# Kernel optimization log

Measured on AMD Instinct MI355X. Metric: run time of the kernel, lower is better.

## Reference

```python
import jax, jax.numpy as jnp
import numpy as np
from jax import lax

B, T, F = 8, 512, 128          # batch, mel time, mel freq
DM, DS, DC, EXP, NL = 384, 16, 4, 2, 12
DI = EXP * DM                   # 768 inner width
DTR = (DM + 15) // 16           # 24, mamba_ssm dt_rank='auto'
PT = PF = 16
L = (T // PT) * (F // PF)       # 256 patches
NC = 4


def setup_inputs() -> dict:
    key = jax.random.key(0)
    ks = iter(jax.random.split(key, 24))
    def n(shape, s=0.02):
        return jax.random.normal(next(ks), shape, jnp.float32) * s
    return {
        "x": jax.random.normal(next(ks), (B, T, F), jnp.float32),
        "patch_w": n((DM, PT, PF)),
        "patch_b": jnp.zeros((DM,), jnp.float32),
        "pos_embed": n((1, L, DM)),
        "ln_g": jnp.ones((NL, DM), jnp.float32),
        "ln_b": jnp.zeros((NL, DM), jnp.float32),
        "in_proj_w": n((NL, 2 * DI, DM)),
        "conv_w": n((NL, DI, DC), 0.1),
        "conv_b": jnp.zeros((NL, DI), jnp.float32),
        "x_proj_w": n((NL, DTR + 2 * DS, DI)),
        "dt_proj_w": n((NL, DI, DTR), 0.1),
        "dt_proj_b": n((NL, DI), 0.1),
        "A_log": jnp.tile(jnp.log(jnp.arange(1, DS + 1, dtype=jnp.float32))[None, None, :], (NL, DI, 1)),
        "Dskip": jnp.ones((NL, DI), jnp.float32),
        "out_proj_w": n((NL, DM, DI)),
        "fn_g": jnp.ones((DM,), jnp.float32),
        "fn_b": jnp.zeros((DM,), jnp.float32),
        "head_w": n((NC, DM)),
        "head_b": jnp.zeros((NC,), jnp.float32),
    }


def _layernorm(x, g, b):
    m = x.mean(-1, keepdims=True)
    v = jnp.var(x, axis=-1, keepdims=True)
    return (x - m) * lax.rsqrt(v + 1e-5) * g + b


def _silu(v):
    return v * jax.nn.sigmoid(v)


def _mamba_block(x, p):
    # x: [B, L, DM]; residual Mamba block (pre-LN, dropout=identity in eval)
    ln_g, ln_b, Wi, cw, cb, Wx, Wdt, bdt, A_log, Dsk, Wo = p
    res = x
    h = _layernorm(x, ln_g, ln_b)
    xz = jnp.einsum('bld,ed->ble', h, Wi)          # [B,L,2*DI]
    u, z = jnp.split(xz, 2, axis=-1)
    # causal depthwise conv1d, kernel DC (small, unrolled)
    up = jnp.pad(u, ((0, 0), (DC - 1, 0), (0, 0)))
    u = sum(up[:, k:k + L, :] * cw[:, k] for k in range(DC)) + cb
    u = _silu(u)
    proj = jnp.einsum('bld,ed->ble', u, Wx)        # [B,L,DTR+2*DS]
    dt, Bm, Cm = jnp.split(proj, [DTR, DTR + DS], axis=-1)
    delta = jax.nn.softplus(jnp.einsum('blr,dr->bld', dt, Wdt) + bdt)  # [B,L,DI]
    A = -jnp.exp(A_log)                            # [DI, DS]
    dA = jnp.exp(delta[..., None] * A)             # [B,L,DI,DS]
    dBu = (delta * u)[..., None] * Bm[:, :, None, :]

    def step(hst, inp):
        dA_t, dBu_t, C_t = inp
        hst = dA_t * hst + dBu_t                   # [B,DI,DS]
        return hst, jnp.einsum('bdn,bn->bd', hst, C_t)

    h0 = jnp.zeros((x.shape[0], DI, DS), x.dtype)
    _, ys = lax.scan(step, h0, (dA.swapaxes(0, 1), dBu.swapaxes(0, 1), Cm.swapaxes(0, 1)))
    y = ys.swapaxes(0, 1) + u * Dsk                # [B,L,DI]
    y = y * _silu(z)
    return res + jnp.einsum('bld,ed->ble', y, Wo)


def reference(x, patch_w, patch_b, pos_embed, ln_g, ln_b, in_proj_w, conv_w, conv_b,
              x_proj_w, dt_proj_w, dt_proj_b, A_log, Dskip, out_proj_w,
              fn_g, fn_b, head_w, head_b):
    Bn = x.shape[0]
    # patch embed = non-overlapping 16x16 conv == blocked reshape + einsum
    patches = x.reshape(Bn, T // PT, PT, F // PF, PF)
    tok = jnp.einsum('bhpwq,dpq->bhwd', patches, patch_w) + patch_b
    tok = tok.reshape(Bn, L, DM) + pos_embed

    def layer(carry, p):
        return _mamba_block(carry, p), None

    tok, _ = lax.scan(layer, tok, (ln_g, ln_b, in_proj_w, conv_w, conv_b,
                                   x_proj_w, dt_proj_w, dt_proj_b, A_log, Dskip, out_proj_w))
    tok = _layernorm(tok, fn_g, fn_b)
    pooled = tok.mean(axis=1)
    return pooled @ head_w.T + head_b
```

## Files before the change

kernel.cpp:

```cpp
#include <hip/hip_runtime.h>
#include <math.h>

namespace {

constexpr int kB   = 8;
constexpr int kL   = 256;
constexpr int kTok = 2048;
constexpr int kDM  = 384;
constexpr int kDI  = 768;
constexpr int kDS  = 16;
constexpr int kDTR = 24;
constexpr int kPROJ = 56;
constexpr int kNL  = 12;

constexpr int kWIN  = 2 * kDI * kDM;
constexpr int kWOUT = kDM * kDI;
constexpr int kWX   = kPROJ * kDI;
constexpr int kWTOT = kWIN + kWOUT + kWX;

typedef float f32x4 __attribute__((ext_vector_type(4)));
typedef short short8 __attribute__((ext_vector_type(8)));

__device__ __forceinline__ float softplus_f(float x) {
  return (x > 20.f) ? x : log1pf(__expf(x));
}
__device__ __forceinline__ float silu_f(float x) {
  return x / (1.f + __expf(-x));
}
__device__ __forceinline__ unsigned short f2bf(float f) {
  union { float f; unsigned u; } v; v.f = f;
  unsigned r = v.u + 0x7FFFu + ((v.u >> 16) & 1u);
  return (unsigned short)(r >> 16);
}
__device__ __forceinline__ float bf2f(unsigned short u) {
  return __uint_as_float((unsigned)u << 16);
}

__global__ __launch_bounds__(256) void patch_gemm_k(
    const float* __restrict__ x, const float* __restrict__ Bw,
    const float* __restrict__ bias, const float* __restrict__ pos,
    float* __restrict__ C) {
  __shared__ float As[16][68];
  __shared__ float Bs[16][68];
  int tid = threadIdx.x;
  int bm = blockIdx.y * 64;
  int bn = blockIdx.x * 64;
  int lr = tid >> 2;
  int lk = (tid & 3) << 2;
  int tm = (tid >> 4) << 2;
  int tn = (tid & 15) << 2;
  float acc[4][4] = {};
  for (int k0 = 0; k0 < 256; k0 += 16) {
    {
      int token = bm + lr;
      int b = token >> 8, l = token & 255;
      int h = l >> 3, w = l & 7;
      int p = k0 >> 4;
      const float* ap = x + ((size_t)(b * 512) + h * 16 + p) * 128 + w * 16 + lk;
      float4 av = *(const float4*)ap;
      As[lk + 0][lr] = av.x; As[lk + 1][lr] = av.y;
      As[lk + 2][lr] = av.z; As[lk + 3][lr] = av.w;
    }
    {
      const float* bp = Bw + (size_t)(bn + lr) * 256 + k0 + lk;
      float4 bv = *(const float4*)bp;
      Bs[lk + 0][lr] = bv.x; Bs[lk + 1][lr] = bv.y;
      Bs[lk + 2][lr] = bv.z; Bs[lk + 3][lr] = bv.w;
    }
    __syncthreads();
    #pragma unroll
    for (int k = 0; k < 16; ++k) {
      float4 a = *(const float4*)&As[k][tm];
      float4 b = *(const float4*)&Bs[k][tn];
      float av[4] = {a.x, a.y, a.z, a.w};
      float bv[4] = {b.x, b.y, b.z, b.w};
      #pragma unroll
      for (int i = 0; i < 4; ++i)
        #pragma unroll
        for (int j = 0; j < 4; ++j)
          acc[i][j] = fmaf(av[i], bv[j], acc[i][j]);
    }
    __syncthreads();
  }
  #pragma unroll
  for (int i = 0; i < 4; ++i) {
    int row = bm + tm + i;
    #pragma unroll
    for (int j = 0; j < 4; ++j) {
      int col = bn + tn + j;
      C[(size_t)row * kDM + col] =
          acc[i][j] + bias[col] + pos[(size_t)(row & 255) * kDM + col];
    }
  }
}

__global__ __launch_bounds__(384) void ln_k(
    const float* __restrict__ in, float* __restrict__ outv,
    const float* __restrict__ g, const float* __restrict__ bb) {
  int t = blockIdx.x, d = threadIdx.x;
  float v = in[(size_t)t * kDM + d];
  float s = v, s2 = v * v;
  #pragma unroll
  for (int m = 32; m >= 1; m >>= 1) {
    s  += __shfl_xor(s, m);
    s2 += __shfl_xor(s2, m);
  }
  __shared__ float ps[6], ps2[6];
  if ((d & 63) == 0) { ps[d >> 6] = s; ps2[d >> 6] = s2; }
  __syncthreads();
  float S = 0.f, S2 = 0.f;
  #pragma unroll
  for (int i = 0; i < 6; ++i) { S += ps[i]; S2 += ps2[i]; }
  float mean = S * (1.f / 384.f);
  float var  = S2 * (1.f / 384.f) - mean * mean;
  float r = rsqrtf(var + 1e-5f);
  outv[(size_t)t * kDM + d] = (v - mean) * r * g[d] + bb[d];
}

__global__ __launch_bounds__(256) void convert_all_k(
    const float* __restrict__ w_in, const float* __restrict__ w_out,
    const float* __restrict__ w_x, unsigned short* __restrict__ dst) {
  int layer = blockIdx.y;
  int i4 = (blockIdx.x * 256 + threadIdx.x) * 4;
  if (i4 >= kWTOT) return;
  const float* src;
  int off;
  if (i4 < kWIN) { src = w_in + (size_t)layer * kWIN; off = i4; }
  else if (i4 < kWIN + kWOUT) { src = w_out + (size_t)layer * kWOUT; off = i4 - kWIN; }
  else { src = w_x + (size_t)layer * kWX; off = i4 - kWIN - kWOUT; }
  float4 v = *(const float4*)(src + off);
  unsigned short o[4] = {f2bf(v.x), f2bf(v.y), f2bf(v.z), f2bf(v.w)};
  *(uint2*)(dst + (size_t)layer * kWTOT + i4) = *(const uint2*)o;
}

__global__ __launch_bounds__(256) void inproj_ln_k(
    const float* __restrict__ tok, const unsigned short* __restrict__ Bw,
    const float* __restrict__ g, const float* __restrict__ bb,
    unsigned short* __restrict__ Cbf, float* __restrict__ proj_zero) {
  __shared__ __align__(16) unsigned short As[4][128][8];
  __shared__ __align__(16) unsigned short Bs[4][128][8];
  __shared__ float smean[128], srstd[128];
  __shared__ float sg_[kDM], sb_[kDM];
  int tid = threadIdx.x;
  int bm = blockIdx.y * 128;
  int bn = blockIdx.x * 128;
  {
    int bid = blockIdx.y * 12 + blockIdx.x;
    for (int i = bid * 256 + tid; i < kTok * kPROJ; i += 192 * 256)
      proj_zero[i] = 0.f;
  }
  for (int i = tid; i < kDM; i += 256) { sg_[i] = g[i]; sb_[i] = bb[i]; }
  {
    int r = tid >> 1, half = tid & 1;
    const float* rp = tok + (size_t)(bm + r) * kDM + half * 192;
    float s = 0.f, s2 = 0.f;
    #pragma unroll
    for (int q = 0; q < 48; ++q) {
      float4 v = ((const float4*)rp)[q];
      s  += v.x + v.y + v.z + v.w;
      s2 += v.x * v.x + v.y * v.y + v.z * v.z + v.w * v.w;
    }
    s  += __shfl_xor(s, 1);
    s2 += __shfl_xor(s2, 1);
    if (half == 0) {
      float mean = s * (1.f / 384.f);
      float var  = s2 * (1.f / 384.f) - mean * mean;
      smean[r] = mean;
      srstd[r] = rsqrtf(var + 1e-5f);
    }
  }
  __syncthreads();
  int wave = tid >> 6, lane = tid & 63;
  int lm = lane & 15, lq = lane >> 4;
  int wm = (wave >> 1) * 64, wn = (wave & 1) * 64;
  f32x4 acc[4][4] = {};
  for (int k0 = 0; k0 < kDM; k0 += 32) {
    int ar0 = tid & 127, aq0 = tid >> 7;
    unsigned short av[2][8];
    float mean = smean[ar0], rstd = srstd[ar0];
    #pragma unroll
    for (int gq = 0; gq < 2; ++gq) {
      int kq = aq0 + gq * 2;
      const float* ap = tok + (size_t)(bm + ar0) * kDM + k0 + kq * 8;
      float4 v0 = ((const float4*)ap)[0];
      float4 v1 = ((const float4*)ap)[1];
      float vv[8] = {v0.x, v0.y, v0.z, v0.w, v1.x, v1.y, v1.z, v1.w};
      #pragma unroll
      for (int j = 0; j < 8; ++j) {
        int k = k0 + kq * 8 + j;
        av[gq][j] = f2bf((vv[j] - mean) * rstd * sg_[k] + sb_[k]);
      }
    }
    uint4 b0 = *(const uint4*)(Bw + (size_t)(bn + ar0) * kDM + k0 + aq0 * 8);
    uint4 b1 = *(const uint4*)(Bw + (size_t)(bn + ar0) * kDM + k0 + (aq0 + 2) * 8);
    __syncthreads();
    *(uint4*)&As[aq0][ar0][0]     = *(const uint4*)av[0];
    *(uint4*)&As[aq0 + 2][ar0][0] = *(const uint4*)av[1];
    *(uint4*)&Bs[aq0][ar0][0]     = b0;
    *(uint4*)&Bs[aq0 + 2][ar0][0] = b1;
    __syncthreads();
    short8 bfrag[4];
    #pragma unroll
    for (int ni = 0; ni < 4; ++ni)
      bfrag[ni] = *(const short8*)&Bs[lq][wn + ni * 16 + lm][0];
    #pragma unroll
    for (int mi = 0; mi < 4; ++mi) {
      short8 afrag = *(const short8*)&As[lq][wm + mi * 16 + lm][0];
      #pragma unroll
      for (int ni = 0; ni < 4; ++ni)
        acc[mi][ni] = __builtin_amdgcn_mfma_f32_16x16x32_bf16(
            afrag, bfrag[ni], acc[mi][ni], 0, 0, 0);
    }
  }
  #pragma unroll
  for (int mi = 0; mi < 4; ++mi) {
    #pragma unroll
    for (int ni = 0; ni < 4; ++ni) {
      int grow0 = bm + wm + mi * 16 + lq * 4;
      int gcol = bn + wn + ni * 16 + lm;
      #pragma unroll
      for (int r = 0; r < 4; ++r)
        Cbf[(size_t)(grow0 + r) * (2 * kDI) + gcol] = f2bf(acc[mi][ni][r]);
    }
  }
}

__global__ __launch_bounds__(256) void xproj_conv_k(
    const unsigned short* __restrict__ xz, const unsigned short* __restrict__ Bw,
    const float* __restrict__ cw, const float* __restrict__ cb,
    float* __restrict__ proj, unsigned short* __restrict__ uT_bf) {
  __shared__ __align__(16) unsigned short As[4][128][8];
  __shared__ __align__(16) unsigned short Bs[4][64][8];
  __shared__ float scw[128][4];
  __shared__ float scb[128];
  int tid = threadIdx.x;
  int bm = blockIdx.x * 128;
  int kbase = blockIdx.y * 128;
  int wave = tid >> 6, lane = tid & 63;
  int lm = lane & 15, lq = lane >> 4;
  int wm = wave * 32;
  f32x4 acc[2][4] = {};

  if (tid < 128) {
    *(float4*)&scw[tid][0] = *(const float4*)(cw + (size_t)(kbase + tid) * 4);
    scb[tid] = cb[kbase + tid];
  }
  __syncthreads();

  int ar0 = tid & 127;
  int aq0 = tid >> 7;
  int t = bm + ar0;
  int b = t >> 8, l = t & 255;

  for (int kt = 0; kt < 4; ++kt) {
    int k0 = kbase + kt * 32;
    unsigned short av[2][8];
    #pragma unroll
    for (int gq = 0; gq < 2; ++gq) {
      int kq = aq0 + gq * 2;
      int dloc = kt * 32 + kq * 8;
      int dg = kbase + dloc;
      float vals[4][8];
      #pragma unroll
      for (int q = 0; q < 4; ++q) {
        if (l - 3 + q >= 0) {
          uint4 r = *(const uint4*)(xz + (size_t)(t - 3 + q) * (2 * kDI) + dg);
          const unsigned short* rs = (const unsigned short*)&r;
          #pragma unroll
          for (int j = 0; j < 8; ++j) vals[q][j] = bf2f(rs[j]);
        } else {
          #pragma unroll
          for (int j = 0; j < 8; ++j) vals[q][j] = 0.f;
        }
      }
      #pragma unroll
      for (int j = 0; j < 8; ++j) {
        float a = scb[dloc + j];
        a = fmaf(vals[0][j], scw[dloc + j][0], a);
        a = fmaf(vals[1][j], scw[dloc + j][1], a);
        a = fmaf(vals[2][j], scw[dloc + j][2], a);
        a = fmaf(vals[3][j], scw[dloc + j][3], a);
        unsigned short ub = f2bf(silu_f(a));
        av[gq][j] = ub;
        uT_bf[((size_t)b * kDI + dg + j) * kL + l] = ub;
      }
    }
    int br0 = tid & 63, bq0 = tid >> 6;
    uint4 b0;
    if (br0 < kPROJ)
      b0 = *(const uint4*)(Bw + (size_t)br0 * kDI + k0 + bq0 * 8);
    else
      b0 = make_uint4(0u, 0u, 0u, 0u);
    __syncthreads();
    *(uint4*)&As[aq0][ar0][0]     = *(const uint4*)av[0];
    *(uint4*)&As[aq0 + 2][ar0][0] = *(const uint4*)av[1];
    *(uint4*)&Bs[bq0][br0][0] = b0;
    __syncthreads();
    short8 bfrag[4];
    #pragma unroll
    for (int ni = 0; ni < 4; ++ni)
      bfrag[ni] = *(const short8*)&Bs[lq][ni * 16 + lm][0];
    #pragma unroll
    for (int mi = 0; mi < 2; ++mi) {
      short8 afrag = *(const short8*)&As[lq][wm + mi * 16 + lm][0];
      #pragma unroll
      for (int ni = 0; ni < 4; ++ni)
        acc[mi][ni] = __builtin_amdgcn_mfma_f32_16x16x32_bf16(
            afrag, bfrag[ni], acc[mi][ni], 0, 0, 0);
    }
  }

  #pragma unroll
  for (int mi = 0; mi < 2; ++mi) {
    #pragma unroll
    for (int ni = 0; ni < 4; ++ni) {
      int grow0 = bm + wm + mi * 16 + lq * 4;
      int gcol = ni * 16 + lm;
      if (gcol < kPROJ) {
        #pragma unroll
        for (int r = 0; r < 4; ++r)
          atomicAdd(&proj[(size_t)(grow0 + r) * kPROJ + gcol], acc[mi][ni][r]);
      }
    }
  }
}

__global__ __launch_bounds__(256) void bgemm_out_k(
    const unsigned short* __restrict__ A, int lda,
    const unsigned short* __restrict__ B, int ldb,
    float* __restrict__ C, int ldc, int Kc) {
  __shared__ __align__(16) unsigned short As[4][128][8];
  __shared__ __align__(16) unsigned short Bs[4][128][8];
  int tid = threadIdx.x;
  int bm = blockIdx.y * 128;
  int bn = blockIdx.x * 128;
  int k_begin = blockIdx.z * Kc;
  int wave = tid >> 6, lane = tid & 63;
  int lm = lane & 15, lq = lane >> 4;
  int wm = (wave >> 1) * 64, wn = (wave & 1) * 64;
  f32x4 acc[4][4] = {};

  for (int kt = 0; kt < Kc; kt += 32) {
    int k0 = k_begin + kt;
    int ar0 = tid & 127, aq0 = tid >> 7;
    int aq1 = aq0 + 2;
    uint4 a0 = *(const uint4*)(A + (size_t)(bm + ar0) * lda + k0 + aq0 * 8);
    uint4 a1 = *(const uint4*)(A + (size_t)(bm + ar0) * lda + k0 + aq1 * 8);
    uint4 b0 = *(const uint4*)(B + (size_t)(bn + ar0) * ldb + k0 + aq0 * 8);
    uint4 b1 = *(const uint4*)(B + (size_t)(bn + ar0) * ldb + k0 + aq1 * 8);
    __syncthreads();
    *(uint4*)&As[aq0][ar0][0] = a0;
    *(uint4*)&As[aq1][ar0][0] = a1;
    *(uint4*)&Bs[aq0][ar0][0] = b0;
    *(uint4*)&Bs[aq1][ar0][0] = b1;
    __syncthreads();
    short8 bfrag[4];
    #pragma unroll
    for (int ni = 0; ni < 4; ++ni)
      bfrag[ni] = *(const short8*)&Bs[lq][wn + ni * 16 + lm][0];
    #pragma unroll
    for (int mi = 0; mi < 4; ++mi) {
      short8 afrag = *(const short8*)&As[lq][wm + mi * 16 + lm][0];
      #pragma unroll
      for (int ni = 0; ni < 4; ++ni)
        acc[mi][ni] = __builtin_amdgcn_mfma_f32_16x16x32_bf16(
            afrag, bfrag[ni], acc[mi][ni], 0, 0, 0);
    }
  }

  #pragma unroll
  for (int mi = 0; mi < 4; ++mi) {
    #pragma unroll
    for (int ni = 0; ni < 4; ++ni) {
      int grow0 = bm + wm + mi * 16 + lq * 4;
      int gcol = bn + wn + ni * 16 + lm;
      #pragma unroll
      for (int r = 0; r < 4; ++r)
        atomicAdd(&C[(size_t)(grow0 + r) * ldc + gcol], acc[mi][ni][r]);
    }
  }
}

__global__ __launch_bounds__(256) void scansplit_k(
    const float* __restrict__ proj, const unsigned short* __restrict__ uT_bf,
    const unsigned short* __restrict__ xz, const float* __restrict__ dtw,
    const float* __restrict__ dtb, const float* __restrict__ A_log,
    const float* __restrict__ Dsk, unsigned short* __restrict__ y_bf) {
  int d0 = blockIdx.x * 8;
  int b = blockIdx.y;
  int tid = threadIdx.x;
  int dsub = tid & 7;
  int nh = (tid >> 3) & 1;
  int c = tid >> 4;
  int d = d0 + dsub;
  __shared__ float sh[16][16][9];
  __shared__ float sca[16][16][9];

  float Av[8];
  {
    const float* ap = A_log + (size_t)d * kDS + nh * 8;
    #pragma unroll
    for (int q = 0; q < 2; ++q) {
      float4 v = ((const float4*)ap)[q];
      Av[q * 4 + 0] = -__expf(v.x);
      Av[q * 4 + 1] = -__expf(v.y);
      Av[q * 4 + 2] = -__expf(v.z);
      Av[q * 4 + 3] = -__expf(v.w);
    }
  }
  float bdt = dtb[d];
  float Dv = Dsk[d];

  const float* pr = proj + ((size_t)(b * kL) + c * 16) * kPROJ;

  float dtlo[8], dthi[8];
  {
    float wdt[24];
    const float* wp = dtw + (size_t)d * kDTR;
    #pragma unroll
    for (int q = 0; q < 6; ++q) {
      float4 v = ((const float4*)wp)[q];
      wdt[q * 4 + 0] = v.x; wdt[q * 4 + 1] = v.y;
      wdt[q * 4 + 2] = v.z; wdt[q * 4 + 3] = v.w;
    }
    const float* prm = pr + (size_t)(nh * 8) * kPROJ;
    float mine[8];
    #pragma unroll
    for (int i = 0; i < 8; ++i) {
      const float* p = prm + (size_t)i * kPROJ;
      float acc = bdt;
      #pragma unroll
      for (int q = 0; q < 6; ++q) {
        float4 v = ((const float4*)p)[q];
        acc = fmaf(v.x, wdt[q * 4 + 0], acc);
        acc = fmaf(v.y, wdt[q * 4 + 1], acc);
        acc = fmaf(v.z, wdt[q * 4 + 2], acc);
        acc = fmaf(v.w, wdt[q * 4 + 3], acc);
      }
      mine[i] = softplus_f(acc);
    }
    #pragma unroll
    for (int i = 0; i < 8; ++i) {
      float other = __shfl_xor(mine[i], 8);
      dtlo[i] = nh ? other : mine[i];
      dthi[i] = nh ? mine[i] : other;
    }
  }

  float u_[16];
  {
    const unsigned short* up = uT_bf + ((size_t)b * kDI + d) * kL + c * 16;
    uint4 v0 = ((const uint4*)up)[0];
    uint4 v1 = ((const uint4*)up)[1];
    const unsigned short* us = (const unsigned short*)&v0;
    #pragma unroll
    for (int i = 0; i < 8; ++i) u_[i] = bf2f(us[i]);
    us = (const unsigned short*)&v1;
    #pragma unroll
    for (int i = 0; i < 8; ++i) u_[8 + i] = bf2f(us[i]);
  }

  float h[8], ca[8];
  #pragma unroll
  for (int n = 0; n < 8; ++n) { h[n] = 0.f; ca[n] = 1.f; }
  #pragma unroll
  for (int i = 0; i < 16; ++i) {
    float dl = (i < 8) ? dtlo[i] : dthi[i - 8];
    float du = dl * u_[i];
    const float* p = pr + (size_t)i * kPROJ + 24 + nh * 8;
    float4 b0 = ((const float4*)p)[0];
    float4 b1 = ((const float4*)p)[1];
    float Bv[8] = {b0.x, b0.y, b0.z, b0.w, b1.x, b1.y, b1.z, b1.w};
    #pragma unroll
    for (int n = 0; n < 8; ++n) {
      float a = __expf(dl * Av[n]);
      h[n] = fmaf(a, h[n], du * Bv[n]);
      ca[n] *= a;
    }
  }
  {
    int nrow = nh * 8;
    #pragma unroll
    for (int q = 0; q < 8; ++q) {
      sh[c][nrow + q][dsub] = h[q];
      sca[c][nrow + q][dsub] = ca[q];
    }
  }
  __syncthreads();

  float h0[8];
  #pragma unroll
  for (int n = 0; n < 8; ++n) h0[n] = 0.f;
  {
    int nrow = nh * 8;
    for (int j = 0; j < c; ++j) {
      #pragma unroll
      for (int q = 0; q < 8; ++q)
        h0[q] = fmaf(sca[j][nrow + q][dsub], h0[q], sh[j][nrow + q][dsub]);
    }
  }

  float sg_[16];
  if (nh == 0) {
    const unsigned short* zp =
        xz + (size_t)(b * kL + c * 16) * (2 * kDI) + kDI + d;
    #pragma unroll
    for (int i = 0; i < 16; ++i)
      sg_[i] = silu_f(bf2f(zp[(size_t)i * (2 * kDI)]));
  }

  unsigned short* yp = y_bf + (size_t)(b * kL + c * 16) * kDI + d;
  #pragma unroll
  for (int i = 0; i < 16; ++i) {
    float dl = (i < 8) ? dtlo[i] : dthi[i - 8];
    float du = dl * u_[i];
    const float* p = pr + (size_t)i * kPROJ + 24 + nh * 8;
    float4 b0 = ((const float4*)p)[0];
    float4 b1 = ((const float4*)p)[1];
    float4 c0 = ((const float4*)(p + 16))[0];
    float4 c1 = ((const float4*)(p + 16))[1];
    float Bv[8] = {b0.x, b0.y, b0.z, b0.w, b1.x, b1.y, b1.z, b1.w};
    float Cv[8] = {c0.x, c0.y, c0.z, c0.w, c1.x, c1.y, c1.z, c1.w};
    float yv = 0.f;
    #pragma unroll
    for (int n = 0; n < 8; ++n) {
      float a = __expf(dl * Av[n]);
      h0[n] = fmaf(a, h0[n], du * Bv[n]);
      yv = fmaf(h0[n], Cv[n], yv);
    }
    yv += __shfl_xor(yv, 8);
    if (nh == 0) yp[(size_t)i * kDI] = f2bf((yv + u_[i] * Dv) * sg_[i]);
  }
}

__global__ __launch_bounds__(384) void pool_k(
    const float* __restrict__ h, float* __restrict__ pooled) {
  int b = blockIdx.x, d = threadIdx.x;
  float acc = 0.f;
  for (int l = 0; l < kL; ++l) acc += h[(size_t)(b * kL + l) * kDM + d];
  pooled[b * kDM + d] = acc * (1.f / 256.f);
}

__global__ __launch_bounds__(64) void head_k(
    const float* __restrict__ pooled, const float* __restrict__ hw,
    const float* __restrict__ hb, float* __restrict__ out) {
  int b = blockIdx.x >> 2, c = blockIdx.x & 3;
  int lane = threadIdx.x;
  float acc = 0.f;
  for (int dd = lane; dd < kDM; dd += 64)
    acc = fmaf(pooled[b * kDM + dd], hw[c * kDM + dd], acc);
  #pragma unroll
  for (int m = 32; m >= 1; m >>= 1) acc += __shfl_xor(acc, m);
  if (lane == 0) out[b * 4 + c] = acc + hb[c];
}

}

extern "C" void kernel_launch(void* const* d_in, const int* in_sizes, int n_in,
                              void* d_out, int out_size, void* d_ws, size_t ws_size,
                              hipStream_t stream) {
  (void)in_sizes; (void)n_in; (void)out_size; (void)ws_size;
  const float* x        = (const float*)d_in[0];
  const float* patch_w  = (const float*)d_in[1];
  const float* patch_b  = (const float*)d_in[2];
  const float* pos      = (const float*)d_in[3];
  const float* ln_g     = (const float*)d_in[4];
  const float* ln_b     = (const float*)d_in[5];
  const float* in_w     = (const float*)d_in[6];
  const float* conv_w   = (const float*)d_in[7];
  const float* conv_b   = (const float*)d_in[8];
  const float* xproj_w  = (const float*)d_in[9];
  const float* dtproj_w = (const float*)d_in[10];
  const float* dtproj_b = (const float*)d_in[11];
  const float* A_log    = (const float*)d_in[12];
  const float* Dskip    = (const float*)d_in[13];
  const float* out_w    = (const float*)d_in[14];
  const float* fn_g     = (const float*)d_in[15];
  const float* fn_b     = (const float*)d_in[16];
  const float* head_w   = (const float*)d_in[17];
  const float* head_b   = (const float*)d_in[18];
  float* out = (float*)d_out;

  float* ws = (float*)d_ws;
  float* tok    = ws; ws += kTok * kDM;
  float* proj   = ws; ws += kTok * kPROJ;
  float* pooled = ws; ws += kB * kDM;
  unsigned short* xz_bf = (unsigned short*)ws; ws += kTok * 2 * kDI / 2;
  unsigned short* uT_bf = (unsigned short*)ws; ws += kTok * kDI / 2;
  unsigned short* y_bf  = (unsigned short*)ws; ws += kTok * kDI / 2;
  unsigned short* w_bf  = (unsigned short*)ws; ws += (size_t)kNL * kWTOT / 2;
  float* lnout = (float*)xz_bf;

  convert_all_k<<<dim3(kWTOT / 4 / 256, kNL), 256, 0, stream>>>(
      in_w, out_w, xproj_w, w_bf);

  patch_gemm_k<<<dim3(6, 32), 256, 0, stream>>>(x, patch_w, patch_b, pos, tok);

  for (int layer = 0; layer < kNL; ++layer) {
    const unsigned short* wl = w_bf + (size_t)layer * kWTOT;
    inproj_ln_k<<<dim3(12, 16), 256, 0, stream>>>(
        tok, wl, ln_g + layer * kDM, ln_b + layer * kDM, xz_bf, proj);
    xproj_conv_k<<<dim3(16, 6), 256, 0, stream>>>(
        xz_bf, wl + kWIN + kWOUT, conv_w + layer * kDI * 4,
        conv_b + layer * kDI, proj, uT_bf);
    scansplit_k<<<dim3(kDI / 8, kB), 256, 0, stream>>>(
        proj, uT_bf, xz_bf, dtproj_w + (size_t)layer * kDI * kDTR,
        dtproj_b + layer * kDI, A_log + (size_t)layer * kDI * kDS,
        Dskip + layer * kDI, y_bf);
    bgemm_out_k<<<dim3(3, 16, 2), 256, 0, stream>>>(
        y_bf, kDI, wl + kWIN, kDI, tok, kDM, kDI / 2);
  }

  ln_k<<<kTok, kDM, 0, stream>>>(tok, lnout, fn_g, fn_b);
  pool_k<<<kB, kDM, 0, stream>>>(lnout, pooled);
  head_k<<<kB * 4, 64, 0, stream>>>(pooled, head_w, head_b, out);
}
```

Baseline: 1.267 ms.

## Halve GEMM M-tiles, raise split-K, fuse final layernorm with mean pooling

Shrinks the M tile of the in-projection and x-projection GEMMs from 128 to 64 rows, doubling their grid sizes so more CUs get work on this small-token problem. The out-projection split-K factor goes from 2 to 4, again to add blocks. The final layernorm now atomically accumulates into the pooled buffer, which is zeroed in the weight-conversion kernel, removing the separate pool kernel and its intermediate buffer. In exchange it does more atomic traffic, re-reads weight tiles more often, and makes the pooled sum order nondeterministic.

```diff
diff --git a/kernel.cpp b/kernel.cpp
--- a/kernel.cpp
+++ b/kernel.cpp
@@ -94,8 +94,8 @@
   }
 }
 
-__global__ __launch_bounds__(384) void ln_k(
-    const float* __restrict__ in, float* __restrict__ outv,
+__global__ __launch_bounds__(384) void lnpool_k(
+    const float* __restrict__ in, float* __restrict__ pooled,
     const float* __restrict__ g, const float* __restrict__ bb) {
   int t = blockIdx.x, d = threadIdx.x;
   float v = in[(size_t)t * kDM + d];
@@ -114,14 +114,20 @@
   float mean = S * (1.f / 384.f);
   float var  = S2 * (1.f / 384.f) - mean * mean;
   float r = rsqrtf(var + 1e-5f);
-  outv[(size_t)t * kDM + d] = (v - mean) * r * g[d] + bb[d];
+  float o = (v - mean) * r * g[d] + bb[d];
+  atomicAdd(&pooled[(size_t)(t >> 8) * kDM + d], o * (1.f / 256.f));
 }
 
 __global__ __launch_bounds__(256) void convert_all_k(
     const float* __restrict__ w_in, const float* __restrict__ w_out,
-    const float* __restrict__ w_x, unsigned short* __restrict__ dst) {
+    const float* __restrict__ w_x, unsigned short* __restrict__ dst,
+    float* __restrict__ pooled_zero) {
   int layer = blockIdx.y;
-  int i4 = (blockIdx.x * 256 + threadIdx.x) * 4;
+  int tid = threadIdx.x;
+  if (layer == 0 && blockIdx.x == 0) {
+    for (int i = tid; i < kB * kDM; i += 256) pooled_zero[i] = 0.f;
+  }
+  int i4 = (blockIdx.x * 256 + tid) * 4;
   if (i4 >= kWTOT) return;
   const float* src;
   int off;
@@ -137,32 +143,32 @@
     const float* __restrict__ tok, const unsigned short* __restrict__ Bw,
     const float* __restrict__ g, const float* __restrict__ bb,
     unsigned short* __restrict__ Cbf, float* __restrict__ proj_zero) {
-  __shared__ __align__(16) unsigned short As[4][128][8];
+  __shared__ __align__(16) unsigned short As[4][64][8];
   __shared__ __align__(16) unsigned short Bs[4][128][8];
-  __shared__ float smean[128], srstd[128];
+  __shared__ float smean[64], srstd[64];
   __shared__ float sg_[kDM], sb_[kDM];
   int tid = threadIdx.x;
-  int bm = blockIdx.y * 128;
+  int bm = blockIdx.y * 64;
   int bn = blockIdx.x * 128;
   {
     int bid = blockIdx.y * 12 + blockIdx.x;
-    for (int i = bid * 256 + tid; i < kTok * kPROJ; i += 192 * 256)
+    for (int i = bid * 256 + tid; i < kTok * kPROJ; i += 384 * 256)
       proj_zero[i] = 0.f;
   }
   for (int i = tid; i < kDM; i += 256) { sg_[i] = g[i]; sb_[i] = bb[i]; }
   {
-    int r = tid >> 1, half = tid & 1;
-    const float* rp = tok + (size_t)(bm + r) * kDM + half * 192;
+    int r = tid >> 2, quarter = tid & 3;
+    const float* rp = tok + (size_t)(bm + r) * kDM + quarter * 96;
     float s = 0.f, s2 = 0.f;
     #pragma unroll
-    for (int q = 0; q < 48; ++q) {
+    for (int q = 0; q < 24; ++q) {
       float4 v = ((const float4*)rp)[q];
       s  += v.x + v.y + v.z + v.w;
       s2 += v.x * v.x + v.y * v.y + v.z * v.z + v.w * v.w;
     }
-    s  += __shfl_xor(s, 1);
-    s2 += __shfl_xor(s2, 1);
-    if (half == 0) {
+    s  += __shfl_xor(s, 1);  s2 += __shfl_xor(s2, 1);
+    s  += __shfl_xor(s, 2);  s2 += __shfl_xor(s2, 2);
+    if (quarter == 0) {
       float mean = s * (1.f / 384.f);
       float var  = s2 * (1.f / 384.f) - mean * mean;
       smean[r] = mean;
@@ -172,39 +178,37 @@
   __syncthreads();
   int wave = tid >> 6, lane = tid & 63;
   int lm = lane & 15, lq = lane >> 4;
-  int wm = (wave >> 1) * 64, wn = (wave & 1) * 64;
-  f32x4 acc[4][4] = {};
+  int wm = (wave & 1) * 32, wn = (wave >> 1) * 64;
+  f32x4 acc[2][4] = {};
   for (int k0 = 0; k0 < kDM; k0 += 32) {
-    int ar0 = tid & 127, aq0 = tid >> 7;
-    unsigned short av[2][8];
-    float mean = smean[ar0], rstd = srstd[ar0];
-    #pragma unroll
-    for (int gq = 0; gq < 2; ++gq) {
-      int kq = aq0 + gq * 2;
-      const float* ap = tok + (size_t)(bm + ar0) * kDM + k0 + kq * 8;
+    int ar = tid & 63, aq = tid >> 6;
+    unsigned short av[8];
+    {
+      float mean = smean[ar], rstd = srstd[ar];
+      const float* ap = tok + (size_t)(bm + ar) * kDM + k0 + aq * 8;
       float4 v0 = ((const float4*)ap)[0];
       float4 v1 = ((const float4*)ap)[1];
       float vv[8] = {v0.x, v0.y, v0.z, v0.w, v1.x, v1.y, v1.z, v1.w};
       #pragma unroll
       for (int j = 0; j < 8; ++j) {
-        int k = k0 + kq * 8 + j;
-        av[gq][j] = f2bf((vv[j] - mean) * rstd * sg_[k] + sb_[k]);
+        int k = k0 + aq * 8 + j;
+        av[j] = f2bf((vv[j] - mean) * rstd * sg_[k] + sb_[k]);
       }
     }
-    uint4 b0 = *(const uint4*)(Bw + (size_t)(bn + ar0) * kDM + k0 + aq0 * 8);
-    uint4 b1 = *(const uint4*)(Bw + (size_t)(bn + ar0) * kDM + k0 + (aq0 + 2) * 8);
-    __syncthreads();
-    *(uint4*)&As[aq0][ar0][0]     = *(const uint4*)av[0];
-    *(uint4*)&As[aq0 + 2][ar0][0] = *(const uint4*)av[1];
-    *(uint4*)&Bs[aq0][ar0][0]     = b0;
-    *(uint4*)&Bs[aq0 + 2][ar0][0] = b1;
+    int br = tid & 127, bq0 = tid >> 7, bq1 = bq0 + 2;
+    uint4 b0 = *(const uint4*)(Bw + (size_t)(bn + br) * kDM + k0 + bq0 * 8);
+    uint4 b1 = *(const uint4*)(Bw + (size_t)(bn + br) * kDM + k0 + bq1 * 8);
+    __syncthreads();
+    *(uint4*)&As[aq][ar][0]  = *(const uint4*)av;
+    *(uint4*)&Bs[bq0][br][0] = b0;
+    *(uint4*)&Bs[bq1][br][0] = b1;
     __syncthreads();
     short8 bfrag[4];
     #pragma unroll
     for (int ni = 0; ni < 4; ++ni)
       bfrag[ni] = *(const short8*)&Bs[lq][wn + ni * 16 + lm][0];
     #pragma unroll
-    for (int mi = 0; mi < 4; ++mi) {
+    for (int mi = 0; mi < 2; ++mi) {
       short8 afrag = *(const short8*)&As[lq][wm + mi * 16 + lm][0];
       #pragma unroll
       for (int ni = 0; ni < 4; ++ni)
@@ -213,7 +217,7 @@
     }
   }
   #pragma unroll
-  for (int mi = 0; mi < 4; ++mi) {
+  for (int mi = 0; mi < 2; ++mi) {
     #pragma unroll
     for (int ni = 0; ni < 4; ++ni) {
       int grow0 = bm + wm + mi * 16 + lq * 4;
@@ -229,17 +233,17 @@
     const unsigned short* __restrict__ xz, const unsigned short* __restrict__ Bw,
     const float* __restrict__ cw, const float* __restrict__ cb,
     float* __restrict__ proj, unsigned short* __restrict__ uT_bf) {
-  __shared__ __align__(16) unsigned short As[4][128][8];
+  __shared__ __align__(16) unsigned short As[4][64][8];
   __shared__ __align__(16) unsigned short Bs[4][64][8];
   __shared__ float scw[128][4];
   __shared__ float scb[128];
   int tid = threadIdx.x;
-  int bm = blockIdx.x * 128;
+  int bm = blockIdx.x * 64;
   int kbase = blockIdx.y * 128;
   int wave = tid >> 6, lane = tid & 63;
   int lm = lane & 15, lq = lane >> 4;
-  int wm = wave * 32;
-  f32x4 acc[2][4] = {};
+  int wm = wave * 16;
+  f32x4 acc[4] = {};
 
   if (tid < 128) {
     *(float4*)&scw[tid][0] = *(const float4*)(cw + (size_t)(kbase + tid) * 4);
@@ -247,19 +251,17 @@
   }
   __syncthreads();
 
-  int ar0 = tid & 127;
-  int aq0 = tid >> 7;
-  int t = bm + ar0;
+  int ar = tid & 63;
+  int aq = tid >> 6;
+  int t = bm + ar;
   int b = t >> 8, l = t & 255;
 
   for (int kt = 0; kt < 4; ++kt) {
     int k0 = kbase + kt * 32;
-    unsigned short av[2][8];
-    #pragma unroll
-    for (int gq = 0; gq < 2; ++gq) {
-      int kq = aq0 + gq * 2;
-      int dloc = kt * 32 + kq * 8;
-      int dg = kbase + dloc;
+    int dloc = kt * 32 + aq * 8;
+    int dg = kbase + dloc;
+    unsigned short av[8];
+    {
       float vals[4][8];
       #pragma unroll
       for (int q = 0; q < 4; ++q) {
@@ -281,46 +283,37 @@
         a = fmaf(vals[2][j], scw[dloc + j][2], a);
         a = fmaf(vals[3][j], scw[dloc + j][3], a);
         unsigned short ub = f2bf(silu_f(a));
-        av[gq][j] = ub;
+        av[j] = ub;
         uT_bf[((size_t)b * kDI + dg + j) * kL + l] = ub;
       }
     }
-    int br0 = tid & 63, bq0 = tid >> 6;
+    int br = tid & 63, bq = tid >> 6;
     uint4 b0;
-    if (br0 < kPROJ)
-      b0 = *(const uint4*)(Bw + (size_t)br0 * kDI + k0 + bq0 * 8);
+    if (br < kPROJ)
+      b0 = *(const uint4*)(Bw + (size_t)br * kDI + k0 + bq * 8);
     else
       b0 = make_uint4(0u, 0u, 0u, 0u);
     __syncthreads();
-    *(uint4*)&As[aq0][ar0][0]     = *(const uint4*)av[0];
-    *(uint4*)&As[aq0 + 2][ar0][0] = *(const uint4*)av[1];
-    *(uint4*)&Bs[bq0][br0][0] = b0;
-    __syncthreads();
-    short8 bfrag[4];
-    #pragma unroll
-    for (int ni = 0; ni < 4; ++ni)
-      bfrag[ni] = *(const short8*)&Bs[lq][ni * 16 + lm][0];
-    #pragma unroll
-    for (int mi = 0; mi < 2; ++mi) {
-      short8 afrag = *(const short8*)&As[lq][wm + mi * 16 + lm][0];
-      #pragma unroll
-      for (int ni = 0; ni < 4; ++ni)
-        acc[mi][ni] = __builtin_amdgcn_mfma_f32_16x16x32_bf16(
-            afrag, bfrag[ni], acc[mi][ni], 0, 0, 0);
-    }
-  }
-
-  #pragma unroll
-  for (int mi = 0; mi < 2; ++mi) {
+    *(uint4*)&As[aq][ar][0] = *(const uint4*)av;
+    *(uint4*)&Bs[bq][br][0] = b0;
+    __syncthreads();
+    short8 afrag = *(const short8*)&As[lq][wm + lm][0];
     #pragma unroll
     for (int ni = 0; ni < 4; ++ni) {
-      int grow0 = bm + wm + mi * 16 + lq * 4;
-      int gcol = ni * 16 + lm;
-      if (gcol < kPROJ) {
-        #pragma unroll
-        for (int r = 0; r < 4; ++r)
-          atomicAdd(&proj[(size_t)(grow0 + r) * kPROJ + gcol], acc[mi][ni][r]);
-      }
+      short8 bfrag = *(const short8*)&Bs[lq][ni * 16 + lm][0];
+      acc[ni] = __builtin_amdgcn_mfma_f32_16x16x32_bf16(
+          afrag, bfrag, acc[ni], 0, 0, 0);
+    }
+  }
+
+  #pragma unroll
+  for (int ni = 0; ni < 4; ++ni) {
+    int grow0 = bm + wm + lq * 4;
+    int gcol = ni * 16 + lm;
+    if (gcol < kPROJ) {
+      #pragma unroll
+      for (int r = 0; r < 4; ++r)
+        atomicAdd(&proj[(size_t)(grow0 + r) * kPROJ + gcol], acc[ni][r]);
     }
   }
 }
@@ -531,14 +524,6 @@
     yv += __shfl_xor(yv, 8);
     if (nh == 0) yp[(size_t)i * kDI] = f2bf((yv + u_[i] * Dv) * sg_[i]);
   }
-}
-
-__global__ __launch_bounds__(384) void pool_k(
-    const float* __restrict__ h, float* __restrict__ pooled) {
-  int b = blockIdx.x, d = threadIdx.x;
-  float acc = 0.f;
-  for (int l = 0; l < kL; ++l) acc += h[(size_t)(b * kL + l) * kDM + d];
-  pooled[b * kDM + d] = acc * (1.f / 256.f);
 }
 
 __global__ __launch_bounds__(64) void head_k(
@@ -589,29 +574,27 @@
   unsigned short* uT_bf = (unsigned short*)ws; ws += kTok * kDI / 2;
   unsigned short* y_bf  = (unsigned short*)ws; ws += kTok * kDI / 2;
   unsigned short* w_bf  = (unsigned short*)ws; ws += (size_t)kNL * kWTOT / 2;
-  float* lnout = (float*)xz_bf;
 
   convert_all_k<<<dim3(kWTOT / 4 / 256, kNL), 256, 0, stream>>>(
-      in_w, out_w, xproj_w, w_bf);
+      in_w, out_w, xproj_w, w_bf, pooled);
 
   patch_gemm_k<<<dim3(6, 32), 256, 0, stream>>>(x, patch_w, patch_b, pos, tok);
 
   for (int layer = 0; layer < kNL; ++layer) {
     const unsigned short* wl = w_bf + (size_t)layer * kWTOT;
-    inproj_ln_k<<<dim3(12, 16), 256, 0, stream>>>(
+    inproj_ln_k<<<dim3(12, 32), 256, 0, stream>>>(
         tok, wl, ln_g + layer * kDM, ln_b + layer * kDM, xz_bf, proj);
-    xproj_conv_k<<<dim3(16, 6), 256, 0, stream>>>(
+    xproj_conv_k<<<dim3(32, 6), 256, 0, stream>>>(
         xz_bf, wl + kWIN + kWOUT, conv_w + layer * kDI * 4,
         conv_b + layer * kDI, proj, uT_bf);
     scansplit_k<<<dim3(kDI / 8, kB), 256, 0, stream>>>(
         proj, uT_bf, xz_bf, dtproj_w + (size_t)layer * kDI * kDTR,
         dtproj_b + layer * kDI, A_log + (size_t)layer * kDI * kDS,
         Dskip + layer * kDI, y_bf);
-    bgemm_out_k<<<dim3(3, 16, 2), 256, 0, stream>>>(
-        y_bf, kDI, wl + kWIN, kDI, tok, kDM, kDI / 2);
-  }
-
-  ln_k<<<kTok, kDM, 0, stream>>>(tok, lnout, fn_g, fn_b);
-  pool_k<<<kB, kDM, 0, stream>>>(lnout, pooled);
+    bgemm_out_k<<<dim3(3, 16, 4), 256, 0, stream>>>(
+        y_bf, kDI, wl + kWIN, kDI, tok, kDM, kDI / 4);
+  }
+
+  lnpool_k<<<kTok, kDM, 0, stream>>>(tok, pooled, fn_g, fn_b);
   head_k<<<kB * 4, 64, 0, stream>>>(pooled, head_w, head_b, out);
 }
```

Measured after the change: 1.147 ms. -9.5%, faster.
